# Optimization experiments

Hardware: AMD Instinct MI355X
Metric: run time of the kernel (lower is better)

The kernel has to match this reference:

```python
import jax, jax.numpy as jnp
import numpy as np

IN_DIM = 784   # 28*28
OUT_DIM = 16
NUM = 5        # grid intervals
K = 3          # spline order
HEADS = 10


def _make_grid():
    # pykan extended grid: linspace(-1,1,NUM+1) extended by K knots on each side
    h = 2.0 / NUM
    pts = np.arange(-K, NUM + K + 1, dtype=np.float32) * h - 1.0  # [NUM+2K+1]=12
    return jnp.asarray(np.broadcast_to(pts, (IN_DIM, pts.shape[0])))


def setup_inputs() -> dict:
    key = jax.random.key(0)
    ks = jax.random.split(key, 6)
    B = 16384
    x = jax.random.normal(ks[0], (B, 1, 28, 28), jnp.float32)
    grid = _make_grid()                                             # [784,12] (buffer)
    coef = jax.random.normal(ks[1], (HEADS, IN_DIM, OUT_DIM, NUM + K), jnp.float32) * 0.1
    scale_base = jax.random.normal(ks[2], (HEADS, IN_DIM, OUT_DIM), jnp.float32) * 0.1
    scale_sp = jnp.ones((HEADS, IN_DIM, OUT_DIM), jnp.float32)
    mask = jnp.ones((HEADS, IN_DIM, OUT_DIM), jnp.float32)
    w1 = jax.random.normal(ks[3], (HEADS, 8, OUT_DIM), jnp.float32) / np.sqrt(OUT_DIM)
    b1 = jnp.zeros((HEADS, 8), jnp.float32)
    w2 = jax.random.normal(ks[4], (HEADS, 1, 8), jnp.float32) / np.sqrt(8.0)
    b2 = jnp.zeros((HEADS, 1), jnp.float32)
    return dict(x=x, grid=grid, coef=coef, scale_base=scale_base, scale_sp=scale_sp,
                mask=mask, w1=w1, b1=b1, w2=w2, b2=b2)


def _b_spline(x, grid, k):
    # x: [B, D], grid: [D, G] -> bases [B, D, G-k-1] (Cox-de Boor recursion, pykan B_batch)
    xg = x[:, :, None]
    g = grid[None]
    B = ((xg >= g[:, :, :-1]) & (xg < g[:, :, 1:])).astype(x.dtype)
    for p in range(1, k + 1):
        left = (xg - g[:, :, :-(p + 1)]) / (g[:, :, p:-1] - g[:, :, :-(p + 1)])
        right = (g[:, :, p + 1:] - xg) / (g[:, :, p + 1:] - g[:, :, 1:-p])
        B = left * B[:, :, :-1] + right * B[:, :, 1:]
    return jnp.nan_to_num(B)


def reference(x, grid, coef, scale_base, scale_sp, mask, w1, b1, w2, b2):
    xf = x.reshape(x.shape[0], -1)                  # [B, 784]
    Bsp = _b_spline(xf, grid, K)                    # [B, 784, NUM+K]
    # KANLayer: y = sum_d mask*(scale_base*silu(x) + scale_sp*spline). Sum over d is
    # linear, so fold (scale_sp*mask) into coef to avoid the [B,H,784,16] intermediate.
    eff_coef = coef * (scale_sp * mask)[..., None]  # [H, 784, 16, NUM+K]
    y_sp = jnp.einsum('bdg,hdog->bho', Bsp, eff_coef)
    y_base = jnp.einsum('bd,hdo->bho', jax.nn.silu(xf), scale_base * mask)
    y = jnp.tanh(y_base + y_sp)                     # [B, H, 16] (nn.Tanh)
    h1 = jnp.tanh(jnp.einsum('bho,hpo->bhp', y, w1) + b1[None])   # Linear(16,8)+Tanh
    out = jnp.einsum('bhp,hqp->bhq', h1, w2) + b2[None]           # Linear(8,1)
    return out[..., 0]                              # concat of 10 heads -> [B, 10]
```

## Files before the change

### kernel.cpp

```cpp
#include <hip/hip_runtime.h>

#define IN_DIM 784
#define NDB 25
#define NUNITS (NDB*9)
#define BATCH 16384
#define NOUTC 160
#define NT16 10
#define HEADS 10
#define KSPLIT 4
#define ROWB 584
#define CHUNKB (64*ROWB)

typedef __attribute__((ext_vector_type(8))) short bf16x8;
typedef __attribute__((ext_vector_type(4))) float f32x4;

__device__ __forceinline__ unsigned short f2bf(float f) {
    unsigned u = __builtin_bit_cast(unsigned, f);
    unsigned r = 0x7FFFu + ((u >> 16) & 1u);
    return (unsigned short)((u + r) >> 16);
}

__global__ void k_wprep(const float* __restrict__ coef, const float* __restrict__ scale_base,
                        const float* __restrict__ scale_sp, const float* __restrict__ mask,
                        unsigned short* __restrict__ Wp) {
    int tid = blockIdx.x * blockDim.x + threadIdx.x;
    if (tid >= NUNITS * 32 * NOUTC) return;
    int frag = tid >> 9;
    int rem  = tid & 511;
    int l = rem >> 3, j = rem & 7;
    int kc = frag / 10, nt = frag - kc * 10;
    int db = kc / 9, c = kc - db * 9;
    int kk = ((l >> 4) << 3) + j;
    int d = db * 32 + kk;
    int n = nt * 16 + (l & 15);
    float v = 0.f;
    if (d < IN_DIM) {
        int h = n >> 4, o = n & 15;
        size_t base = ((size_t)h * IN_DIM + d) * 16 + o;
        float m = mask[base];
        v = (c == 0) ? scale_base[base] * m
                     : coef[base * 8 + (c - 1)] * scale_sp[base] * m * 0.16666667f;
    }
    Wp[tid] = f2bf(v);
}

__global__ void __launch_bounds__(512, 4) k_fused(const float* __restrict__ x,
                                                  const float* __restrict__ gridp,
                                                  const unsigned short* __restrict__ Wp,
                                                  float* __restrict__ part) {
    __shared__ char ldsb[CHUNKB];
    const int tid = threadIdx.x;
    const int l = tid & 63, wid = tid >> 6;
    const int rr = l & 15, q = l >> 4;
    const int rg = wid >> 1, nh = wid & 1;
    const int sd = tid & 31, srg = tid >> 5;
    const int row0g = blockIdx.x * 64;
    const int y = blockIdx.y;
    const int db0 = (y * NDB) >> 2, db1 = ((y + 1) * NDB) >> 2;

    const float g0 = gridp[0];
    const float ih = 1.f / (gridp[1] - g0);
    const float nihg0 = -g0 * ih;

    f32x4 acc[5];
    #pragma unroll
    for (int i = 0; i < 5; ++i) acc[i] = (f32x4){0.f, 0.f, 0.f, 0.f};

    const char* wpb = (const char*)Wp;
    float xv[4];

    auto loadX = [&](int db) {
        const int d = db * 32 + sd;
        const int dc = d < IN_DIM ? d : IN_DIM - 1;
        const float* xp = x + (size_t)(row0g + srg) * IN_DIM + dc;
        #pragma unroll
        for (int it = 0; it < 4; ++it) xv[it] = xp[(size_t)it * 16 * IN_DIM];
    };

    auto evalScatter = [&]() {
        #pragma unroll
        for (int it = 0; it < 4; ++it) {
            const float v = xv[it];
            const float u = fmaf(v, ih, nihg0);
            const float fm = floorf(u);
            const int m = (int)fm;
            const float t = u - fm;
            const float t2 = t * t;
            const float w0 = t2 * t;
            const float w1 = fmaf(fmaf(fmaf(-3.f, t, 3.f), t, 3.f), t, 1.f);
            const float w2 = fmaf(fmaf(3.f, t, -6.f) * t, t, 4.f);
            const float omt = 1.f - t;
            const float w3 = omt * omt * omt;
            const float den = 1.f + __expf(-v);
            float inv; asm("v_rcp_f32 %0, %1" : "=v"(inv) : "v"(den));
            const float sil = v * inv;
            char* rb = ldsb + (it * 16 + srg) * ROWB + sd * 2;
            *(unsigned short*)rb = f2bf(sil);
            #pragma unroll
            for (int s = 0; s < 8; ++s) {
                const int ms = m - s;
                const unsigned off = (((unsigned)ms & 7u) << 6) + 64u;
                float wv = 0.f;
                if (s <= 3) {
                    const float wsel = (s == 0) ? w0 : (s == 1) ? w1 : (s == 2) ? w2 : w3;
                    wv = ((unsigned)ms <= 7u) ? wsel : 0.f;
                }
                *(unsigned short*)(rb + off) = f2bf(wv);
            }
        }
    };

    loadX(db0);
    for (int db = db0; db < db1; ++db) {
        __syncthreads();
        evalScatter();
        if (db + 1 < db1) loadX(db + 1);
        __syncthreads();

        const char* arow = ldsb + (rg * 16 + rr) * ROWB + q * 16;
        const char* bb = wpb + (size_t)db * 92160 + nh * 5120 + l * 16;
        #pragma unroll
        for (int c = 0; c < 9; ++c) {
            const bf16x8 a = *(const bf16x8*)(arow + c * 64);
            const char* bc = bb + c * 10240;
            const bf16x8 b0 = *(const bf16x8*)(bc);
            const bf16x8 b1 = *(const bf16x8*)(bc + 1024);
            const bf16x8 b2 = *(const bf16x8*)(bc + 2048);
            const bf16x8 b3 = *(const bf16x8*)(bc + 3072);
            const bf16x8 b4 = *(const bf16x8*)(bc + 4096);
            acc[0] = __builtin_amdgcn_mfma_f32_16x16x32_bf16(a, b0, acc[0], 0, 0, 0);
            acc[1] = __builtin_amdgcn_mfma_f32_16x16x32_bf16(a, b1, acc[1], 0, 0, 0);
            acc[2] = __builtin_amdgcn_mfma_f32_16x16x32_bf16(a, b2, acc[2], 0, 0, 0);
            acc[3] = __builtin_amdgcn_mfma_f32_16x16x32_bf16(a, b3, acc[3], 0, 0, 0);
            acc[4] = __builtin_amdgcn_mfma_f32_16x16x32_bf16(a, b4, acc[4], 0, 0, 0);
        }
    }

    float* pp = part + (size_t)y * BATCH * NOUTC;
    #pragma unroll
    for (int ntl = 0; ntl < 5; ++ntl) {
        const int col = (nh * 5 + ntl) * 16 + rr;
        #pragma unroll
        for (int ii = 0; ii < 4; ++ii)
            pp[(size_t)(row0g + rg * 16 + q * 4 + ii) * NOUTC + col] = acc[ntl][ii];
    }
}

__global__ void k_epi(const float* __restrict__ part, const float* __restrict__ w1,
                      const float* __restrict__ b1, const float* __restrict__ w2,
                      const float* __restrict__ b2, float* __restrict__ out) {
    int t = blockIdx.x * blockDim.x + threadIdx.x;
    if (t >= BATCH * HEADS) return;
    int b = t / HEADS;
    int h = t - b * HEADS;
    const f32x4* P = (const f32x4*)part;
    const int vbase = b * (NOUTC / 4) + h * 4;
    float y[16];
    #pragma unroll
    for (int c4 = 0; c4 < 4; ++c4) {
        f32x4 v = P[vbase + c4];
        #pragma unroll
        for (int s = 1; s < KSPLIT; ++s) {
            f32x4 v2 = P[(size_t)s * BATCH * (NOUTC / 4) + vbase + c4];
            v.x += v2.x; v.y += v2.y; v.z += v2.z; v.w += v2.w;
        }
        y[c4 * 4 + 0] = tanhf(v.x); y[c4 * 4 + 1] = tanhf(v.y);
        y[c4 * 4 + 2] = tanhf(v.z); y[c4 * 4 + 3] = tanhf(v.w);
    }
    float oacc = b2[h];
    #pragma unroll
    for (int p = 0; p < 8; ++p) {
        float a = b1[h * 8 + p];
        const float* wr = w1 + ((size_t)h * 8 + p) * 16;
        #pragma unroll
        for (int o = 0; o < 16; ++o) a = fmaf(y[o], wr[o], a);
        oacc = fmaf(tanhf(a), w2[h * 8 + p], oacc);
    }
    out[t] = oacc;
}

extern "C" void kernel_launch(void* const* d_in, const int* in_sizes, int n_in,
                              void* d_out, int out_size, void* d_ws, size_t ws_size,
                              hipStream_t stream) {
    const float* x          = (const float*)d_in[0];
    const float* gridp      = (const float*)d_in[1];
    const float* coef       = (const float*)d_in[2];
    const float* scale_base = (const float*)d_in[3];
    const float* scale_sp   = (const float*)d_in[4];
    const float* mask       = (const float*)d_in[5];
    const float* w1         = (const float*)d_in[6];
    const float* b1         = (const float*)d_in[7];
    const float* w2         = (const float*)d_in[8];
    const float* b2         = (const float*)d_in[9];
    float* out = (float*)d_out;

    char* ws = (char*)d_ws;
    float* part        = (float*)ws;
    unsigned short* Wp = (unsigned short*)(ws + 41943040);

    k_wprep<<<dim3((NUNITS * 32 * NOUTC + 255) / 256), dim3(256), 0, stream>>>(coef, scale_base, scale_sp, mask, Wp);
    k_fused<<<dim3(BATCH / 64, KSPLIT), dim3(512), 0, stream>>>(x, gridp, Wp, part);
    k_epi  <<<dim3((BATCH * HEADS + 255) / 256), dim3(256), 0, stream>>>(part, w1, b1, w2, b2, out);
}
```

Baseline: 129.3 us.

## Double row tile per block, reuse B fragments across two row groups, prefetch B

Each block now processes 128 batch rows instead of 64, so every wave computes two 16-row tiles and reuses each loaded weight fragment for two MFMAs, halving global weight traffic per output. Weight fragments for the next k-chunk are software-prefetched into registers, and bf16 packing uses the hardware v_cvt_pk_bf16_f32 instruction instead of manual rounding. LDS use doubles to about 75KB per block and register pressure rises, which can cut occupancy, and the grid shrinks to half as many blocks.

Result: faster. 121.5 us (-6.0%).

```diff
diff --git a/kernel.cpp b/kernel.cpp
--- a/kernel.cpp
+++ b/kernel.cpp
@@ -5,11 +5,11 @@
 #define NUNITS (NDB*9)
 #define BATCH 16384
 #define NOUTC 160
-#define NT16 10
 #define HEADS 10
 #define KSPLIT 4
+#define MROWS 128
 #define ROWB 584
-#define CHUNKB (64*ROWB)
+#define CHUNKB (MROWS*ROWB)
 
 typedef __attribute__((ext_vector_type(8))) short bf16x8;
 typedef __attribute__((ext_vector_type(4))) float f32x4;
@@ -52,9 +52,9 @@
     const int tid = threadIdx.x;
     const int l = tid & 63, wid = tid >> 6;
     const int rr = l & 15, q = l >> 4;
-    const int rg = wid >> 1, nh = wid & 1;
+    const int rp = wid >> 1, nh = wid & 1;
     const int sd = tid & 31, srg = tid >> 5;
-    const int row0g = blockIdx.x * 64;
+    const int row0g = blockIdx.x * MROWS;
     const int y = blockIdx.y;
     const int db0 = (y * NDB) >> 2, db1 = ((y + 1) * NDB) >> 2;
 
@@ -62,24 +62,27 @@
     const float ih = 1.f / (gridp[1] - g0);
     const float nihg0 = -g0 * ih;
 
-    f32x4 acc[5];
-    #pragma unroll
-    for (int i = 0; i < 5; ++i) acc[i] = (f32x4){0.f, 0.f, 0.f, 0.f};
+    f32x4 acc[2][5];
+    #pragma unroll
+    for (int rg = 0; rg < 2; ++rg)
+        #pragma unroll
+        for (int i = 0; i < 5; ++i) acc[rg][i] = (f32x4){0.f, 0.f, 0.f, 0.f};
 
     const char* wpb = (const char*)Wp;
-    float xv[4];
+    float xv[8];
 
     auto loadX = [&](int db) {
         const int d = db * 32 + sd;
         const int dc = d < IN_DIM ? d : IN_DIM - 1;
         const float* xp = x + (size_t)(row0g + srg) * IN_DIM + dc;
         #pragma unroll
-        for (int it = 0; it < 4; ++it) xv[it] = xp[(size_t)it * 16 * IN_DIM];
+        for (int it = 0; it < 8; ++it) xv[it] = xp[(size_t)it * 16 * IN_DIM];
     };
 
     auto evalScatter = [&]() {
-        #pragma unroll
-        for (int it = 0; it < 4; ++it) {
+        char* rb0 = ldsb + srg * ROWB + sd * 2;
+        #pragma unroll
+        for (int it = 0; it < 8; ++it) {
             const float v = xv[it];
             const float u = fmaf(v, ih, nihg0);
             const float fm = floorf(u);
@@ -94,55 +97,69 @@
             const float den = 1.f + __expf(-v);
             float inv; asm("v_rcp_f32 %0, %1" : "=v"(inv) : "v"(den));
             const float sil = v * inv;
-            char* rb = ldsb + (it * 16 + srg) * ROWB + sd * 2;
-            *(unsigned short*)rb = f2bf(sil);
+            unsigned p01, p23, ps;
+            asm("v_cvt_pk_bf16_f32 %0, %1, %2" : "=v"(p01) : "v"(w0), "v"(w1));
+            asm("v_cvt_pk_bf16_f32 %0, %1, %2" : "=v"(p23) : "v"(w2), "v"(w3));
+            asm("v_cvt_pk_bf16_f32 %0, %1, %2" : "=v"(ps)  : "v"(sil), "v"(sil));
+            const unsigned h1 = p01 >> 16, h3 = p23 >> 16;
+            char* rb = rb0 + it * 16 * ROWB;
+            *(unsigned short*)rb = (unsigned short)ps;
             #pragma unroll
             for (int s = 0; s < 8; ++s) {
                 const int ms = m - s;
-                const unsigned off = (((unsigned)ms & 7u) << 6) + 64u;
-                float wv = 0.f;
+                unsigned wv = 0u;
                 if (s <= 3) {
-                    const float wsel = (s == 0) ? w0 : (s == 1) ? w1 : (s == 2) ? w2 : w3;
-                    wv = ((unsigned)ms <= 7u) ? wsel : 0.f;
+                    const unsigned wsel = (s == 0) ? p01 : (s == 1) ? h1 : (s == 2) ? p23 : h3;
+                    wv = ((unsigned)ms <= 7u) ? wsel : 0u;
                 }
-                *(unsigned short*)(rb + off) = f2bf(wv);
+                *(unsigned short*)(rb + (((unsigned)ms & 7u) << 6) + 64) = (unsigned short)wv;
             }
         }
     };
 
     loadX(db0);
+    #pragma unroll 1
     for (int db = db0; db < db1; ++db) {
         __syncthreads();
         evalScatter();
         if (db + 1 < db1) loadX(db + 1);
         __syncthreads();
 
-        const char* arow = ldsb + (rg * 16 + rr) * ROWB + q * 16;
+        const char* arow = ldsb + (rp * 32 + rr) * ROWB + q * 16;
         const char* bb = wpb + (size_t)db * 92160 + nh * 5120 + l * 16;
+        bf16x8 bn[5];
+        #pragma unroll
+        for (int nt = 0; nt < 5; ++nt) bn[nt] = *(const bf16x8*)(bb + nt * 1024);
         #pragma unroll
         for (int c = 0; c < 9; ++c) {
-            const bf16x8 a = *(const bf16x8*)(arow + c * 64);
-            const char* bc = bb + c * 10240;
-            const bf16x8 b0 = *(const bf16x8*)(bc);
-            const bf16x8 b1 = *(const bf16x8*)(bc + 1024);
-            const bf16x8 b2 = *(const bf16x8*)(bc + 2048);
-            const bf16x8 b3 = *(const bf16x8*)(bc + 3072);
-            const bf16x8 b4 = *(const bf16x8*)(bc + 4096);
-            acc[0] = __builtin_amdgcn_mfma_f32_16x16x32_bf16(a, b0, acc[0], 0, 0, 0);
-            acc[1] = __builtin_amdgcn_mfma_f32_16x16x32_bf16(a, b1, acc[1], 0, 0, 0);
-            acc[2] = __builtin_amdgcn_mfma_f32_16x16x32_bf16(a, b2, acc[2], 0, 0, 0);
-            acc[3] = __builtin_amdgcn_mfma_f32_16x16x32_bf16(a, b3, acc[3], 0, 0, 0);
-            acc[4] = __builtin_amdgcn_mfma_f32_16x16x32_bf16(a, b4, acc[4], 0, 0, 0);
+            bf16x8 bc[5];
+            #pragma unroll
+            for (int nt = 0; nt < 5; ++nt) bc[nt] = bn[nt];
+            if (c < 8) {
+                const char* bnx = bb + (c + 1) * 10240;
+                #pragma unroll
+                for (int nt = 0; nt < 5; ++nt) bn[nt] = *(const bf16x8*)(bnx + nt * 1024);
+            }
+            const bf16x8 a0 = *(const bf16x8*)(arow + c * 64);
+            const bf16x8 a1 = *(const bf16x8*)(arow + 16 * ROWB + c * 64);
+            #pragma unroll
+            for (int nt = 0; nt < 5; ++nt) {
+                acc[0][nt] = __builtin_amdgcn_mfma_f32_16x16x32_bf16(a0, bc[nt], acc[0][nt], 0, 0, 0);
+                acc[1][nt] = __builtin_amdgcn_mfma_f32_16x16x32_bf16(a1, bc[nt], acc[1][nt], 0, 0, 0);
+            }
         }
     }
 
     float* pp = part + (size_t)y * BATCH * NOUTC;
     #pragma unroll
-    for (int ntl = 0; ntl < 5; ++ntl) {
-        const int col = (nh * 5 + ntl) * 16 + rr;
-        #pragma unroll
-        for (int ii = 0; ii < 4; ++ii)
-            pp[(size_t)(row0g + rg * 16 + q * 4 + ii) * NOUTC + col] = acc[ntl][ii];
+    for (int rg = 0; rg < 2; ++rg) {
+        #pragma unroll
+        for (int ntl = 0; ntl < 5; ++ntl) {
+            const int col = (nh * 5 + ntl) * 16 + rr;
+            #pragma unroll
+            for (int ii = 0; ii < 4; ++ii)
+                pp[(size_t)(row0g + (rp * 2 + rg) * 16 + q * 4 + ii) * NOUTC + col] = acc[rg][ntl][ii];
+        }
     }
 }
 
@@ -199,6 +216,6 @@
     unsigned short* Wp = (unsigned short*)(ws + 41943040);
 
     k_wprep<<<dim3((NUNITS * 32 * NOUTC + 255) / 256), dim3(256), 0, stream>>>(coef, scale_base, scale_sp, mask, Wp);
-    k_fused<<<dim3(BATCH / 64, KSPLIT), dim3(512), 0, stream>>>(x, gridp, Wp, part);
+    k_fused<<<dim3(BATCH / MROWS, KSPLIT), dim3(512), 0, stream>>>(x, gridp, Wp, part);
     k_epi  <<<dim3((BATCH * HEADS + 255) / 256), dim3(256), 0, stream>>>(part, w1, b1, w2, b2, out);
 }
```
